# Performance work log

Hardware: AMD Instinct MI355X
Metric: run time of the kernel (lower is better)

## Reference

```python
import jax, jax.numpy as jnp
import numpy as np

N_NODES = 50000
N_EDGES = 800000
NODE = 64
EDGE = 32
READOUT = 256
DEPTH = 4
NUM_GRAPHS = 512
BN_EPS = 1e-5

# Assumption (ffn / hidden_xavier_bn not in source): ffn = Linear + ReLU;
# hidden_xavier_bn = Linear -> BatchNorm (batch stats) -> ReLU.

def _ffn(h, W, b):
    return jax.nn.relu(h @ W + b)

def setup_inputs() -> dict:
    key = jax.random.key(0)
    ks = jax.random.split(key, 16)
    def lin(k, fin, fout):
        return jax.random.normal(k, (fin, fout), jnp.float32) / np.sqrt(fin)
    inp = {
        "x": jax.random.normal(ks[0], (N_NODES, NODE), jnp.float32),
        "edge_index": jax.random.randint(ks[1], (2, N_EDGES), 0, N_NODES),
        "edge_attr": jax.random.normal(ks[2], (N_EDGES, EDGE), jnp.float32),
        "w_atoms": jax.random.uniform(ks[3], (N_NODES,), jnp.float32),
        "w_bonds": jax.random.uniform(ks[4], (N_EDGES,), jnp.float32),
        "batch": jnp.sort(jax.random.randint(ks[5], (N_NODES,), 0, NUM_GRAPHS)),
        "V_W": lin(ks[6], NODE, NODE), "V_b": jnp.zeros((NODE,), jnp.float32),
        "E_W": lin(ks[7], EDGE, EDGE), "E_b": jnp.zeros((EDGE,), jnp.float32),
        "U_W": lin(ks[8], 2 * NODE + EDGE, NODE), "U_b": jnp.zeros((NODE,), jnp.float32),
        "R_W": lin(ks[9], NODE, READOUT), "R_b": jnp.zeros((READOUT,), jnp.float32),
        "R_gamma": jnp.ones((READOUT,), jnp.float32),
        "R_beta": jnp.zeros((READOUT,), jnp.float32),
    }
    return inp


def reference(x, edge_index, edge_attr, w_atoms, w_bonds, batch,
              V_W, V_b, E_W, E_b, U_W, U_b, R_W, R_b, R_gamma, R_beta):
    src, dst = edge_index[0], edge_index[1]  # x_j = x[src], aggregate at dst
    x_clone = x  # .clone().detach()

    # Edge FFN output is loop-invariant (same edge_attr each depth)
    m_ij = _ffn(edge_attr, E_W, E_b)  # [E, EDGE]

    def mp(h):
        m_j = _ffn(h[src], V_W, V_b)                              # [E, NODE]
        msg = w_bonds[:, None] * jnp.concatenate([m_j, m_ij], 1)  # [E, NODE+EDGE]
        aggr = jax.ops.segment_sum(msg, dst, num_segments=N_NODES)
        up = jax.nn.elu(jnp.concatenate([aggr, h], 1))            # [N, 2*NODE+EDGE]
        return _ffn(up, U_W, U_b) * w_atoms[:, None]              # [N, NODE]

    h = x
    last_x = None
    last_last_x = None
    for i in range(DEPTH):
        if i == 0 or i == 1:
            h = mp(h)
        else:
            h = mp(last_last_x + h)
        if i > 0:
            last_last_x = last_x
        last_x = h

    # Readout: Linear -> BatchNorm(batch stats) -> ReLU
    y = (h + x_clone) @ R_W + R_b
    mu = jnp.mean(y, axis=0)
    var = jnp.var(y, axis=0)
    y = jax.nn.relu((y - mu) * jax.lax.rsqrt(var + BN_EPS) * R_gamma + R_beta)

    # normalize_embedding=True -> scatter_mean over graphs
    sums = jax.ops.segment_sum(y, batch, num_segments=NUM_GRAPHS)
    cnts = jax.ops.segment_sum(jnp.ones((N_NODES,), y.dtype), batch,
                               num_segments=NUM_GRAPHS)
    return sums / jnp.maximum(cnts, 1.0)[:, None]
```

## Files before the change

### kernel.cpp

```cpp
#include <hip/hip_runtime.h>
#include <hip/hip_fp16.h>
#include <cstdint>
#include <cstddef>

#define NODE 64
#define EDGEF 32
#define UPF 160
#define RD 256
#define UT_STRIDE 162

__device__ __forceinline__ float eluf(float x) { return x > 0.f ? x : expm1f(x); }

union U32H2 { unsigned int u; __half2 h; };
union H16U { __half h; unsigned short u; };

__device__ __forceinline__ float2 h2f(unsigned int u) {
    U32H2 t; t.u = u;
    return __half22float2(t.h);
}
__device__ __forceinline__ unsigned short f2h(float f) {
    H16U t; t.h = __float2half_rn(f);
    return t.u;
}

__global__ void k_count(const int* __restrict__ dst, int* cnt, int E) {
    int e = blockIdx.x * 256 + threadIdx.x;
    if (e < E) atomicAdd(&cnt[dst[e]], 1);
}

__global__ void k_scanA(const int* __restrict__ cnt, int* starts, int* bsum, int N) {
    __shared__ int sh[256];
    int t = threadIdx.x;
    int base = blockIdx.x * 1024 + t * 4;
    int v0 = 0, v1 = 0, v2 = 0, v3 = 0;
    if (base + 0 < N) v0 = cnt[base + 0];
    if (base + 1 < N) v1 = cnt[base + 1];
    if (base + 2 < N) v2 = cnt[base + 2];
    if (base + 3 < N) v3 = cnt[base + 3];
    int tot = v0 + v1 + v2 + v3;
    sh[t] = tot;
    __syncthreads();
    for (int off = 1; off < 256; off <<= 1) {
        int add = (t >= off) ? sh[t - off] : 0;
        __syncthreads();
        sh[t] += add;
        __syncthreads();
    }
    int excl = sh[t] - tot;
    if (base + 0 < N) starts[base + 0] = excl;
    if (base + 1 < N) starts[base + 1] = excl + v0;
    if (base + 2 < N) starts[base + 2] = excl + v0 + v1;
    if (base + 3 < N) starts[base + 3] = excl + v0 + v1 + v2;
    if (t == 255) bsum[blockIdx.x] = sh[255];
}

__global__ void k_scanB(const int* __restrict__ bsum, int* boff, int nb, int* starts, int N) {
    if (threadIdx.x == 0 && blockIdx.x == 0) {
        int run = 0;
        for (int b = 0; b < nb; ++b) { boff[b] = run; run += bsum[b]; }
        starts[N] = run;
    }
}

__global__ void k_scanC(const int* __restrict__ boff, int* starts, int* cursor, int N) {
    int i = blockIdx.x * 256 + threadIdx.x;
    if (i < N) {
        int v = starts[i] + boff[i >> 10];
        starts[i] = v;
        cursor[i] = v;
    }
}

__global__ void k_fill(const int* __restrict__ src, const int* __restrict__ dst,
                       const float* __restrict__ wb, int* cursor,
                       int* esrc, float* ewS, int* eidx, int E) {
    int e = blockIdx.x * 256 + threadIdx.x;
    if (e < E) {
        int pos = atomicAdd(&cursor[dst[e]], 1);
        esrc[pos] = src[e];
        ewS[pos] = wb[e];
        eidx[pos] = e;
    }
}

__global__ __launch_bounds__(256, 6) void k_aggrE(
    const float* __restrict__ eattr, const int* __restrict__ eidx,
    const float* __restrict__ ewS, const int* __restrict__ starts,
    const float* __restrict__ EW, const float* __restrict__ Eb,
    float* __restrict__ aggrE_elu, int N) {
    __shared__ float slot[4][2][EDGEF];
    int tid = threadIdx.x;
    int lane = tid & 63, wid = tid >> 6;
    int half = lane >> 5, ch = lane & 31;
    float ewcol[EDGEF];
#pragma unroll
    for (int k = 0; k < EDGEF; ++k) ewcol[k] = EW[k * EDGEF + ch];
    float eb = Eb[ch];
    float* myslot = slot[wid][half];
    const float4* s4 = (const float4*)myslot;
    int nwaves = gridDim.x * 4;
    for (int n = blockIdx.x * 4 + wid; n < N; n += nwaves) {
        int s0 = starts[n], s1 = starts[n + 1];
        float acc = 0.f;
        int i = s0 + half;
        float a0 = 0.f, a1 = 0.f, a2 = 0.f, a3 = 0.f;
        if (i     < s1) a0 = eattr[(size_t)eidx[i]     * EDGEF + ch];
        if (i + 2 < s1) a1 = eattr[(size_t)eidx[i + 2] * EDGEF + ch];
        if (i + 4 < s1) a2 = eattr[(size_t)eidx[i + 4] * EDGEF + ch];
        if (i + 6 < s1) a3 = eattr[(size_t)eidx[i + 6] * EDGEF + ch];
        for (; i < s1; i += 2) {
            float aN = 0.f;
            if (i + 8 < s1) aN = eattr[(size_t)eidx[i + 8] * EDGEF + ch];
            myslot[ch] = a0;
            float m0 = eb, m1 = 0.f;
#pragma unroll
            for (int q = 0; q < 8; ++q) {
                float4 a4 = s4[q];
                m0 = fmaf(a4.x, ewcol[4*q+0], m0);
                m1 = fmaf(a4.y, ewcol[4*q+1], m1);
                m0 = fmaf(a4.z, ewcol[4*q+2], m0);
                m1 = fmaf(a4.w, ewcol[4*q+3], m1);
            }
            acc = fmaf(ewS[i], fmaxf(m0 + m1, 0.f), acc);
            a0 = a1; a1 = a2; a2 = a3; a3 = aN;
        }
        acc += __shfl_xor(acc, 32, 64);
        if (lane < EDGEF) aggrE_elu[(size_t)n * EDGEF + lane] = eluf(acc);
    }
}

__global__ __launch_bounds__(256) void k_hv(
    const float* __restrict__ ha, const float* __restrict__ hb, int addB,
    const float* __restrict__ VW, const float* __restrict__ Vb,
    unsigned short* __restrict__ hvh, int N, int chunk) {
    __shared__ float slot[4][NODE];
    int tid = threadIdx.x;
    int lane = tid & 63, w = tid >> 6;
    float vcol[NODE];
#pragma unroll
    for (int k = 0; k < NODE; ++k) vcol[k] = VW[k * NODE + lane];
    float vb = Vb[lane];
    const float4* s4 = (const float4*)slot[w];
    int n0 = blockIdx.x * chunk;
    int n1 = n0 + chunk; if (n1 > N) n1 = N;
    for (int n = n0 + w; n < n1; n += 4) {
        float hrow = ha[(size_t)n * NODE + lane];
        if (addB) hrow += hb[(size_t)n * NODE + lane];
        slot[w][lane] = hrow;
        float d0 = 0.f, d1 = 0.f, d2 = 0.f, d3 = 0.f;
#pragma unroll
        for (int q = 0; q < 16; ++q) {
            float4 h4 = s4[q];
            d0 = fmaf(h4.x, vcol[4*q+0], d0);
            d1 = fmaf(h4.y, vcol[4*q+1], d1);
            d2 = fmaf(h4.z, vcol[4*q+2], d2);
            d3 = fmaf(h4.w, vcol[4*q+3], d3);
        }
        hvh[(size_t)n * NODE + lane] = f2h(fmaxf(vb + ((d0 + d1) + (d2 + d3)), 0.f));
    }
}

__global__ __launch_bounds__(512, 8) void k_gather(
    const unsigned short* __restrict__ hvh, const int* __restrict__ starts,
    const int* __restrict__ esrc, const float* __restrict__ ewS,
    float* __restrict__ aggr, int N) {
    int lane = threadIdx.x & 63, wid = threadIdx.x >> 6;
    int grp = lane >> 4, gl = lane & 15;
    int nwaves = gridDim.x * 8;
    for (int n = blockIdx.x * 8 + wid; n < N; n += nwaves) {
        int s0 = starts[n], s1 = starts[n + 1];
        int deg = s1 - s0;
        float4 acc = {0.f, 0.f, 0.f, 0.f};
        uint2 r0 = {0u, 0u}, r1 = {0u, 0u}, r2 = {0u, 0u};
        float w0 = 0.f, w1 = 0.f, w2 = 0.f;
        if (grp < deg) {
            r0 = *(const uint2*)(hvh + (size_t)esrc[s0 + grp] * NODE + gl * 4);
            w0 = ewS[s0 + grp];
        }
        if (grp + 4 < deg) {
            r1 = *(const uint2*)(hvh + (size_t)esrc[s0 + grp + 4] * NODE + gl * 4);
            w1 = ewS[s0 + grp + 4];
        }
        if (grp + 8 < deg) {
            r2 = *(const uint2*)(hvh + (size_t)esrc[s0 + grp + 8] * NODE + gl * 4);
            w2 = ewS[s0 + grp + 8];
        }
        for (int i = grp; i < deg; i += 4) {
            uint2 rN = {0u, 0u}; float wN = 0.f;
            if (i + 12 < deg) {
                rN = *(const uint2*)(hvh + (size_t)esrc[s0 + i + 12] * NODE + gl * 4);
                wN = ewS[s0 + i + 12];
            }
            float2 f0 = h2f(r0.x), f1 = h2f(r0.y);
            acc.x = fmaf(w0, f0.x, acc.x);
            acc.y = fmaf(w0, f0.y, acc.y);
            acc.z = fmaf(w0, f1.x, acc.z);
            acc.w = fmaf(w0, f1.y, acc.w);
            r0 = r1; w0 = w1;
            r1 = r2; w1 = w2;
            r2 = rN; w2 = wN;
        }
        acc.x += __shfl_xor(acc.x, 16, 64);
        acc.y += __shfl_xor(acc.y, 16, 64);
        acc.z += __shfl_xor(acc.z, 16, 64);
        acc.w += __shfl_xor(acc.w, 16, 64);
        acc.x += __shfl_xor(acc.x, 32, 64);
        acc.y += __shfl_xor(acc.y, 32, 64);
        acc.z += __shfl_xor(acc.z, 32, 64);
        acc.w += __shfl_xor(acc.w, 32, 64);
        if (lane < 16)
            *(float4*)(aggr + (size_t)n * NODE + gl * 4) = acc;
    }
}

__global__ __launch_bounds__(512, 4) void k_update(
    const float* __restrict__ ha, const float* __restrict__ hb, int addB,
    const float* __restrict__ aggr, const float* __restrict__ aggrE_elu,
    const float* __restrict__ UW, const float* __restrict__ Ub,
    const float* __restrict__ watoms, float* __restrict__ h_out, int N) {
    __shared__ float lds_Ut[NODE * UT_STRIDE];
    __shared__ float lds_up[8 * UPF];
    int tid = threadIdx.x;
    for (int idx = tid; idx < UPF * NODE; idx += 512) {
        int j = idx & 63, t2 = idx >> 6;
        lds_Ut[j * UT_STRIDE + t2] = UW[idx];
    }
    int lane = tid & 63, wid = tid >> 6;
    float ub = Ub[lane];
    __syncthreads();
    float* myup = lds_up + wid * UPF;
    int nwaves = gridDim.x * 8;
    for (int n = blockIdx.x * 8 + wid; n < N; n += nwaves) {
        myup[lane] = eluf(aggr[(size_t)n * NODE + lane]);
        if (lane < EDGEF) myup[NODE + lane] = aggrE_elu[(size_t)n * EDGEF + lane];
        float hrow = ha[(size_t)n * NODE + lane];
        if (addB) hrow += hb[(size_t)n * NODE + lane];
        myup[NODE + EDGEF + lane] = eluf(hrow);
        float o = ub;
#pragma unroll
        for (int t2 = 0; t2 < UPF; t2 += 2) {
            float2 u2 = *(const float2*)&myup[t2];
            float2 w2 = *(const float2*)&lds_Ut[lane * UT_STRIDE + t2];
            o = fmaf(u2.x, w2.x, o);
            o = fmaf(u2.y, w2.y, o);
        }
        h_out[(size_t)n * NODE + lane] = fmaxf(o, 0.f) * watoms[n];
    }
}

__global__ __launch_bounds__(256) void k_y(
    const float* __restrict__ ha, const float* __restrict__ hb,
    const float* __restrict__ RW, const float* __restrict__ Rb,
    float* __restrict__ y, float* colsum, float* colsumsq, int N, int chunk) {
    __shared__ float slot[4][NODE];
    int tid = threadIdx.x;
    int lane = tid & 63, w = tid >> 6;
    float rcol[NODE];
#pragma unroll
    for (int k = 0; k < NODE; ++k) rcol[k] = RW[k * RD + w * 64 + lane];
    float rb = Rb[w * 64 + lane];
    const float4* s4 = (const float4*)slot[w];
    float sum = 0.f, sq = 0.f;
    int n0 = blockIdx.x * chunk;
    int n1 = n0 + chunk; if (n1 > N) n1 = N;
    for (int n = n0; n < n1; ++n) {
        float hvC = ha[(size_t)n * NODE + lane] + hb[(size_t)n * NODE + lane];
        slot[w][lane] = hvC;
        float d0 = 0.f, d1 = 0.f, d2 = 0.f, d3 = 0.f;
#pragma unroll
        for (int q = 0; q < 16; ++q) {
            float4 h4 = s4[q];
            d0 = fmaf(h4.x, rcol[4*q+0], d0);
            d1 = fmaf(h4.y, rcol[4*q+1], d1);
            d2 = fmaf(h4.z, rcol[4*q+2], d2);
            d3 = fmaf(h4.w, rcol[4*q+3], d3);
        }
        float v = rb + ((d0 + d1) + (d2 + d3));
        y[(size_t)n * RD + w * 64 + lane] = v;
        sum += v; sq = fmaf(v, v, sq);
    }
    atomicAdd(&colsum[w * 64 + lane], sum);
    atomicAdd(&colsumsq[w * 64 + lane], sq);
}

__global__ void k_gbounds(const int* __restrict__ batch, int* gstart, int N, int G) {
    int n = blockIdx.x * 256 + threadIdx.x;
    if (n > N) return;
    int bprev = (n == 0) ? -1 : batch[n - 1];
    int bcur = (n == N) ? G : batch[n];
    for (int g = bprev + 1; g <= bcur; ++g) gstart[g] = n;
}

__global__ void k_out(const float* __restrict__ y, const float* __restrict__ colsum,
                      const float* __restrict__ colsumsq, const float* __restrict__ gamma,
                      const float* __restrict__ beta, const int* __restrict__ gstart,
                      float* __restrict__ out, float invN) {
    int g = blockIdx.x, c = threadIdx.x;
    float mu = colsum[c] * invN;
    float var = fmaxf(colsumsq[c] * invN - mu * mu, 0.f);
    float inv = rsqrtf(var + 1e-5f);
    float ga = gamma[c], be = beta[c];
    int a = gstart[g], b = gstart[g + 1];
    float acc = 0.f;
    for (int n = a; n < b; ++n) {
        float v = y[(size_t)n * RD + c];
        acc += fmaxf(fmaf((v - mu) * inv, ga, be), 0.f);
    }
    out[(size_t)g * RD + c] = acc / fmaxf((float)(b - a), 1.f);
}

extern "C" void kernel_launch(void* const* d_in, const int* in_sizes, int n_in,
                              void* d_out, int out_size, void* d_ws, size_t ws_size,
                              hipStream_t stream) {
    const float* x      = (const float*)d_in[0];
    const int*   ei     = (const int*)d_in[1];
    const float* eattr  = (const float*)d_in[2];
    const float* watoms = (const float*)d_in[3];
    const float* wbonds = (const float*)d_in[4];
    const int*   batch  = (const int*)d_in[5];
    const float* VW = (const float*)d_in[6];
    const float* Vb = (const float*)d_in[7];
    const float* EW = (const float*)d_in[8];
    const float* Eb = (const float*)d_in[9];
    const float* UW = (const float*)d_in[10];
    const float* Ub = (const float*)d_in[11];
    const float* RW = (const float*)d_in[12];
    const float* Rb = (const float*)d_in[13];
    const float* Rg = (const float*)d_in[14];
    const float* Rbe = (const float*)d_in[15];
    float* out = (float*)d_out;

    const int N = in_sizes[0] / NODE;
    const int E = in_sizes[4];
    const int G = out_size / RD;
    const int* src = ei;
    const int* dst = ei + E;

    char* p = (char*)d_ws;
    auto alloc = [&](size_t bytes) -> char* {
        char* r = p;
        p += (bytes + 255) & ~(size_t)255;
        return r;
    };
    float* aggrE   = (float*)alloc((size_t)N * EDGEF * 4);
    int*   cnt     = (int*)alloc((size_t)N * 4);
    int*   starts  = (int*)alloc((size_t)(N + 1) * 4);
    int*   cursor  = (int*)alloc((size_t)N * 4);
    int*   bsum    = (int*)alloc(64 * 4);
    int*   boff    = (int*)alloc(64 * 4);
    int*   esrc    = (int*)alloc((size_t)E * 4);
    float* ewS     = (float*)alloc((size_t)E * 4);
    int*   eidx    = (int*)alloc((size_t)E * 4);
    float* hA      = (float*)alloc((size_t)N * NODE * 4);
    float* hB      = (float*)alloc((size_t)N * NODE * 4);
    unsigned short* hvh = (unsigned short*)alloc((size_t)N * NODE * 2);
    float* aggr    = (float*)alloc((size_t)N * NODE * 4);
    float* colstat = (float*)alloc((size_t)2 * RD * 4);
    int*   gstart  = (int*)alloc((size_t)(G + 1) * 4);
    float* ybuf    = (float*)alloc((size_t)N * RD * 4);

    hipMemsetAsync(cnt, 0, (size_t)N * 4, stream);
    hipMemsetAsync(colstat, 0, (size_t)2 * RD * 4, stream);

    int eblocks = (E + 255) / 256;
    int sblocks = (N + 1023) / 1024;

    k_count<<<eblocks, 256, 0, stream>>>(dst, cnt, E);
    k_scanA<<<sblocks, 256, 0, stream>>>(cnt, starts, bsum, N);
    k_scanB<<<1, 64, 0, stream>>>(bsum, boff, sblocks, starts, N);
    k_scanC<<<(N + 255) / 256, 256, 0, stream>>>(boff, starts, cursor, N);
    k_fill<<<eblocks, 256, 0, stream>>>(src, dst, wbonds, cursor, esrc, ewS, eidx, E);
    k_aggrE<<<2048, 256, 0, stream>>>(eattr, eidx, ewS, starts, EW, Eb, aggrE, N);

    int hvblocks = 512;
    int chunk = (N + hvblocks - 1) / hvblocks;

    k_hv<<<hvblocks, 256, 0, stream>>>(x, x, 0, VW, Vb, hvh, N, chunk);
    k_gather<<<2048, 512, 0, stream>>>(hvh, starts, esrc, ewS, aggr, N);
    k_update<<<768, 512, 0, stream>>>(x, x, 0, aggr, aggrE, UW, Ub, watoms, hA, N);
    k_hv<<<hvblocks, 256, 0, stream>>>(hA, hA, 0, VW, Vb, hvh, N, chunk);
    k_gather<<<2048, 512, 0, stream>>>(hvh, starts, esrc, ewS, aggr, N);
    k_update<<<768, 512, 0, stream>>>(hA, hA, 0, aggr, aggrE, UW, Ub, watoms, hB, N);
    k_hv<<<hvblocks, 256, 0, stream>>>(hA, hB, 1, VW, Vb, hvh, N, chunk);
    k_gather<<<2048, 512, 0, stream>>>(hvh, starts, esrc, ewS, aggr, N);
    k_update<<<768, 512, 0, stream>>>(hA, hB, 1, aggr, aggrE, UW, Ub, watoms, hA, N);
    k_hv<<<hvblocks, 256, 0, stream>>>(hB, hA, 1, VW, Vb, hvh, N, chunk);
    k_gather<<<2048, 512, 0, stream>>>(hvh, starts, esrc, ewS, aggr, N);
    k_update<<<768, 512, 0, stream>>>(hB, hA, 1, aggr, aggrE, UW, Ub, watoms, hB, N);

    k_y<<<512, 256, 0, stream>>>(hB, x, RW, Rb, ybuf, colstat, colstat + RD, N, chunk);
    k_gbounds<<<(N + 256) / 256, 256, 0, stream>>>(batch, gstart, N, G);
    k_out<<<G, RD, 0, stream>>>(ybuf, colstat, colstat + RD, Rg, Rbe, gstart, out, 1.0f / (float)N);
}
```

Measured before the change: 684.7 us.

## Fuse edge FFN into CSR fill and sum precomputed fp16 messages per node

The edge-feature FFN is now computed once per edge in edge order, with coalesced reads of edge_attr, inside the CSR fill kernel. The weighted fp16 result is written at the sorted CSR position, which replaces the eidx indirection and the random gathers of edge_attr in the aggregation kernel. A new light kernel sums the fp16 messages per destination node and applies ELU. The change adds a 51 MB fp16 scratch buffer that aliases ybuf, trades fp32 for fp16 precision in the edge messages, and makes the fill kernel's writes scattered.

```diff
diff --git a/kernel.cpp b/kernel.cpp
--- a/kernel.cpp
+++ b/kernel.cpp
@@ -71,61 +71,87 @@
     }
 }
 
-__global__ void k_fill(const int* __restrict__ src, const int* __restrict__ dst,
-                       const float* __restrict__ wb, int* cursor,
-                       int* esrc, float* ewS, int* eidx, int E) {
-    int e = blockIdx.x * 256 + threadIdx.x;
-    if (e < E) {
-        int pos = atomicAdd(&cursor[dst[e]], 1);
-        esrc[pos] = src[e];
-        ewS[pos] = wb[e];
-        eidx[pos] = e;
-    }
-}
-
-__global__ __launch_bounds__(256, 6) void k_aggrE(
-    const float* __restrict__ eattr, const int* __restrict__ eidx,
-    const float* __restrict__ ewS, const int* __restrict__ starts,
-    const float* __restrict__ EW, const float* __restrict__ Eb,
+__global__ void k_fill_mij(const float* __restrict__ ea, const int* __restrict__ src,
+                           const int* __restrict__ dst, const float* __restrict__ wb,
+                           const float* __restrict__ EW, const float* __restrict__ Eb,
+                           int* cursor, int* esrc, float* ewS,
+                           unsigned short* __restrict__ medge, int E) {
+    __shared__ float ew_s[EDGEF * EDGEF];
+    __shared__ float eb_s[EDGEF];
+    int tid = threadIdx.x;
+    for (int i = tid; i < EDGEF * EDGEF; i += 256) ew_s[i] = EW[i];
+    if (tid < EDGEF) eb_s[tid] = Eb[tid];
+    __syncthreads();
+    int e = blockIdx.x * 256 + tid;
+    if (e >= E) return;
+    float a[EDGEF];
+    const float4* row = (const float4*)(ea + (size_t)e * EDGEF);
+#pragma unroll
+    for (int q = 0; q < 8; ++q) {
+        float4 v = row[q];
+        a[4*q] = v.x; a[4*q+1] = v.y; a[4*q+2] = v.z; a[4*q+3] = v.w;
+    }
+    float m[EDGEF];
+#pragma unroll
+    for (int j = 0; j < EDGEF; ++j) m[j] = eb_s[j];
+#pragma unroll
+    for (int k = 0; k < EDGEF; ++k) {
+        float ak = a[k];
+#pragma unroll
+        for (int j = 0; j < EDGEF; ++j) m[j] = fmaf(ak, ew_s[k*EDGEF + j], m[j]);
+    }
+    float w = wb[e];
+    int pos = atomicAdd(&cursor[dst[e]], 1);
+    esrc[pos] = src[e];
+    ewS[pos] = w;
+    uint4 pk[4];
+    unsigned int* pu = (unsigned int*)pk;
+#pragma unroll
+    for (int q = 0; q < 8; ++q) {
+        unsigned int h0 = f2h(w * fmaxf(m[4*q+0], 0.f));
+        unsigned int h1 = f2h(w * fmaxf(m[4*q+1], 0.f));
+        unsigned int h2 = f2h(w * fmaxf(m[4*q+2], 0.f));
+        unsigned int h3 = f2h(w * fmaxf(m[4*q+3], 0.f));
+        pu[2*q]   = h0 | (h1 << 16);
+        pu[2*q+1] = h2 | (h3 << 16);
+    }
+    uint4* mp = (uint4*)(medge + (size_t)pos * EDGEF);
+    mp[0] = pk[0];
+    mp[1] = pk[1];
+    mp[2] = pk[2];
+    mp[3] = pk[3];
+}
+
+__global__ __launch_bounds__(256) void k_sumE(
+    const unsigned short* __restrict__ medge, const int* __restrict__ starts,
     float* __restrict__ aggrE_elu, int N) {
-    __shared__ float slot[4][2][EDGEF];
     int tid = threadIdx.x;
     int lane = tid & 63, wid = tid >> 6;
-    int half = lane >> 5, ch = lane & 31;
-    float ewcol[EDGEF];
-#pragma unroll
-    for (int k = 0; k < EDGEF; ++k) ewcol[k] = EW[k * EDGEF + ch];
-    float eb = Eb[ch];
-    float* myslot = slot[wid][half];
-    const float4* s4 = (const float4*)myslot;
+    int grp = lane >> 4, gl = lane & 15;
+    const unsigned int* m32 = (const unsigned int*)medge;
     int nwaves = gridDim.x * 4;
     for (int n = blockIdx.x * 4 + wid; n < N; n += nwaves) {
         int s0 = starts[n], s1 = starts[n + 1];
-        float acc = 0.f;
-        int i = s0 + half;
-        float a0 = 0.f, a1 = 0.f, a2 = 0.f, a3 = 0.f;
-        if (i     < s1) a0 = eattr[(size_t)eidx[i]     * EDGEF + ch];
-        if (i + 2 < s1) a1 = eattr[(size_t)eidx[i + 2] * EDGEF + ch];
-        if (i + 4 < s1) a2 = eattr[(size_t)eidx[i + 4] * EDGEF + ch];
-        if (i + 6 < s1) a3 = eattr[(size_t)eidx[i + 6] * EDGEF + ch];
-        for (; i < s1; i += 2) {
-            float aN = 0.f;
-            if (i + 8 < s1) aN = eattr[(size_t)eidx[i + 8] * EDGEF + ch];
-            myslot[ch] = a0;
-            float m0 = eb, m1 = 0.f;
-#pragma unroll
-            for (int q = 0; q < 8; ++q) {
-                float4 a4 = s4[q];
-                m0 = fmaf(a4.x, ewcol[4*q+0], m0);
-                m1 = fmaf(a4.y, ewcol[4*q+1], m1);
-                m0 = fmaf(a4.z, ewcol[4*q+2], m0);
-                m1 = fmaf(a4.w, ewcol[4*q+3], m1);
-            }
-            acc = fmaf(ewS[i], fmaxf(m0 + m1, 0.f), acc);
-            a0 = a1; a1 = a2; a2 = a3; a3 = aN;
-        }
-        acc += __shfl_xor(acc, 32, 64);
-        if (lane < EDGEF) aggrE_elu[(size_t)n * EDGEF + lane] = eluf(acc);
+        float2 acc = {0.f, 0.f};
+        int i = s0 + grp;
+        unsigned int r0 = 0u;
+        if (i < s1) r0 = m32[(size_t)i * 16 + gl];
+        for (; i < s1; i += 4) {
+            unsigned int rN = 0u;
+            if (i + 4 < s1) rN = m32[(size_t)(i + 4) * 16 + gl];
+            float2 f = h2f(r0);
+            acc.x += f.x;
+            acc.y += f.y;
+            r0 = rN;
+        }
+        acc.x += __shfl_xor(acc.x, 16, 64);
+        acc.y += __shfl_xor(acc.y, 16, 64);
+        acc.x += __shfl_xor(acc.x, 32, 64);
+        acc.y += __shfl_xor(acc.y, 32, 64);
+        if (lane < 16) {
+            float2 o = { eluf(acc.x), eluf(acc.y) };
+            *(float2*)(aggrE_elu + (size_t)n * EDGEF + 2 * gl) = o;
+        }
     }
 }
 
@@ -350,14 +376,16 @@
     int*   boff    = (int*)alloc(64 * 4);
     int*   esrc    = (int*)alloc((size_t)E * 4);
     float* ewS     = (float*)alloc((size_t)E * 4);
-    int*   eidx    = (int*)alloc((size_t)E * 4);
     float* hA      = (float*)alloc((size_t)N * NODE * 4);
     float* hB      = (float*)alloc((size_t)N * NODE * 4);
     unsigned short* hvh = (unsigned short*)alloc((size_t)N * NODE * 2);
     float* aggr    = (float*)alloc((size_t)N * NODE * 4);
     float* colstat = (float*)alloc((size_t)2 * RD * 4);
     int*   gstart  = (int*)alloc((size_t)(G + 1) * 4);
-    float* ybuf    = (float*)alloc((size_t)N * RD * 4);
+    size_t mbytes = (size_t)E * EDGEF * 2;
+    size_t ybytes = (size_t)N * RD * 4;
+    float* ybuf = (float*)alloc(mbytes > ybytes ? mbytes : ybytes);
+    unsigned short* medge = (unsigned short*)ybuf;
 
     hipMemsetAsync(cnt, 0, (size_t)N * 4, stream);
     hipMemsetAsync(colstat, 0, (size_t)2 * RD * 4, stream);
@@ -369,8 +397,9 @@
     k_scanA<<<sblocks, 256, 0, stream>>>(cnt, starts, bsum, N);
     k_scanB<<<1, 64, 0, stream>>>(bsum, boff, sblocks, starts, N);
     k_scanC<<<(N + 255) / 256, 256, 0, stream>>>(boff, starts, cursor, N);
-    k_fill<<<eblocks, 256, 0, stream>>>(src, dst, wbonds, cursor, esrc, ewS, eidx, E);
-    k_aggrE<<<2048, 256, 0, stream>>>(eattr, eidx, ewS, starts, EW, Eb, aggrE, N);
+    k_fill_mij<<<eblocks, 256, 0, stream>>>(eattr, src, dst, wbonds, EW, Eb,
+                                            cursor, esrc, ewS, medge, E);
+    k_sumE<<<2048, 256, 0, stream>>>(medge, starts, aggrE, N);
 
     int hvblocks = 512;
     int chunk = (N + hvblocks - 1) / hvblocks;
```

Result: no change. 698.2 us (+2.0%).
